# Optimization experiments

Measured on AMD Instinct MI355X. Metric: run time of the kernel, lower is better.

The kernel has to match this reference:

```python
import jax, jax.numpy as jnp
import numpy as np

PC = 512      # proposal_channels == conv_channels
INCH = 512    # in_channels of branch
B = 8
T = 64        # pyramid level length (feat_t) at order=0
TF = 256      # frame_level_feature length (clip_length)
KERNELS = [8, 16, 8, 4, 2, 2, 2]  # ConPoolingKernal
CLC = 498     # feature_lastclass channels (CLC + 2 == 500)
GROUPS = 32


def _gn(x, gamma, beta):
    # GroupNorm(32, C) over [B, C, L]
    Bb, C, L = x.shape
    xg = x.reshape(Bb, GROUPS, C // GROUPS, L)
    m = xg.mean(axis=(2, 3), keepdims=True)
    v = xg.var(axis=(2, 3), keepdims=True)
    xn = ((xg - m) * jax.lax.rsqrt(v + 1e-5)).reshape(Bb, C, L)
    return xn * gamma[None, :, None] + beta[None, :, None]


def _c1(x, w, b):
    # Unit1D kernel_shape=1: pointwise conv
    return jnp.einsum('bct,oc->bot', x, w) + b[None, :, None]


def _bmp(feat, segs):
    # BoundaryMaxPooling: first C/2 channels max-pooled over segs[...,0:2],
    # second C/2 over segs[...,2:4] (inclusive integer ranges, clamped).
    Bb, C, L = feat.shape
    C2 = C // 2
    pos = jnp.arange(L)
    def pool(f, s, e):
        s = jnp.clip(s, 0, L - 1)
        e = jnp.maximum(jnp.clip(e, 0, L - 1), s)
        mask = (pos[None, None, :] >= s[..., None]) & (pos[None, None, :] <= e[..., None])  # [B,T,L]
        return jnp.max(jnp.where(mask[:, None], f[:, :, None, :], -jnp.inf), axis=-1)  # [B,C2,T]
    return jnp.concatenate([pool(feat[:, :C2], segs[..., 0], segs[..., 1]),
                            pool(feat[:, C2:], segs[..., 2], segs[..., 3])], axis=1)


def _anchor_gather(feat, anc, K):
    # Vectorized per-anchor clamp/slice + nearest F.interpolate(size=K):
    # src index for output k of a slice [l, r] is l + floor(k * (r - l + 1) / K).
    Bb, C, L = feat.shape
    left = jnp.clip(anc[..., 0], 0, L)
    right = jnp.clip(anc[..., 1], 0, L)
    valid = right > left                      # empty slices -> zeros (torch branch)
    seglen = right + 1 - left
    k = jnp.arange(K)
    idx = jnp.clip(left[..., None] + (k[None, None, :] * seglen[..., None]) // K, 0, L - 1)  # [B,T,K]
    g = jax.vmap(lambda f, ix: f[:, ix])(feat, idx)   # [B,C,T,K]
    return g * valid[:, None, :, None].astype(feat.dtype)


def setup_inputs() -> dict:
    key = jax.random.key(0)
    ks = jax.random.split(key, 16)
    f32 = jnp.float32
    s = 0.02
    def w(k, shape):
        return jax.random.normal(k, shape, f32) * s
    inp = {}
    inp['feature'] = jax.random.normal(ks[0], (B, INCH, T), f32)
    inp['frame_level_feature'] = jax.random.normal(ks[1], (B, PC, TF), f32)
    inp['segments'] = jax.random.randint(ks[2], (B, T, 4), 0, T).astype(jnp.int32)
    inp['frame_segments'] = jax.random.randint(ks[3], (B, T, 4), 0, TF).astype(jnp.int32)
    inp['feature_lastclass'] = jax.random.normal(ks[4], (B, CLC, T), f32)
    inp['anchor'] = jnp.sort(jax.random.randint(ks[5], (B, T, 2), 0, T), axis=-1).astype(jnp.int32)
    inp['frame_anchor'] = jnp.sort(jax.random.randint(ks[6], (B, T, 2), 0, TF), axis=-1).astype(jnp.int32)
    inp['order'] = 0
    inp['LocResult_feature'] = jax.random.normal(ks[7], (B, 2, T), f32)
    inp['w_cur'] = w(ks[8], (PC, INCH)); inp['b_cur'] = jnp.zeros((PC,), f32)
    inp['g_cur'] = jnp.ones((PC,), f32); inp['be_cur'] = jnp.zeros((PC,), f32)
    inp['w_lr'] = w(ks[9], (2 * PC, INCH)); inp['b_lr'] = jnp.zeros((2 * PC,), f32)
    inp['g_lr'] = jnp.ones((2 * PC,), f32); inp['be_lr'] = jnp.zeros((2 * PC,), f32)
    inp['w_roi'] = w(ks[10], (PC, PC)); inp['b_roi'] = jnp.zeros((PC,), f32)
    inp['g_roi'] = jnp.ones((PC,), f32); inp['be_roi'] = jnp.zeros((PC,), f32)
    K1 = KERNELS[1]; K0 = KERNELS[0]
    inp['w_cp'] = w(ks[11], (PC, 2 * PC, K1)); inp['b_cp'] = jnp.zeros((PC,), f32)
    inp['w_cp0'] = w(ks[12], (PC, PC, K0)); inp['b_cp0'] = jnp.zeros((PC,), f32)
    CIN = 6 * PC + 500
    inp['w_prop'] = w(ks[13], (INCH, CIN)); inp['b_prop'] = jnp.zeros((INCH,), f32)
    inp['g_prop'] = jnp.ones((INCH,), f32); inp['be_prop'] = jnp.zeros((INCH,), f32)
    return inp


def reference(feature, frame_level_feature, segments, frame_segments, feature_lastclass,
              anchor, frame_anchor, order, LocResult_feature,
              w_cur, b_cur, g_cur, be_cur, w_lr, b_lr, g_lr, be_lr,
              w_roi, b_roi, g_roi, be_roi, w_cp, b_cp, w_cp0, b_cp0,
              w_prop, b_prop, g_prop, be_prop):
    relu = jax.nn.relu
    fm_short = relu(_gn(_c1(feature, w_cur, b_cur), g_cur, be_cur))           # [B,PC,T]
    feat_lr = relu(_gn(_c1(feature, w_lr, b_lr), g_lr, be_lr))                # [B,2PC,T]
    prop_feature = _bmp(feat_lr, segments)                                    # [B,2PC,T]
    prop_roi = relu(_gn(_c1(_bmp(frame_level_feature, frame_segments), w_roi, b_roi), g_roi, be_roi))
    K1 = KERNELS[order + 1]
    K0 = KERNELS[0]
    g1 = _anchor_gather(feat_lr, anchor, K1)                                  # [B,2PC,T,K1]
    con_feature = jnp.einsum('bctk,ock->bot', g1, w_cp) + b_cp[None, :, None]  # valid conv K1->1
    g0 = _anchor_gather(frame_level_feature, frame_anchor, K0)                # [B,PC,T,K0]
    frame_con = jnp.einsum('bctk,ock->bot', g0, w_cp0) + b_cp0[None, :, None]
    prop_con = relu(_gn(_c1(frame_con, w_roi, b_roi), g_roi, be_roi))
    cat = jnp.concatenate([prop_roi, prop_feature, fm_short, feature_lastclass,
                           con_feature, prop_con, LocResult_feature], axis=1)  # [B,6PC+500,T]
    out = relu(_gn(_c1(cat, w_prop, b_prop), g_prop, be_prop))                # [B,INCH,T]
    return (out, feat_lr)
```

## Files before the change

kernel.cpp:

```cpp
#include <hip/hip_runtime.h>
#include <math.h>

#define BB 8
#define CATP 3584
#define CAT_REAL 3572

typedef __attribute__((ext_vector_type(8))) short short8;
typedef __attribute__((ext_vector_type(4))) float f32x4;

__device__ inline ushort f2bf(float f) {
  union { float f; unsigned u; } x;
  x.f = f;
  return (ushort)((x.u + 0x7FFFu + ((x.u >> 16) & 1u)) >> 16);
}
__device__ inline float bf2f(unsigned us) {
  union { unsigned u; float f; } x;
  x.u = us << 16;
  return x.f;
}

__global__ __launch_bounds__(256) void cvt_weights_kernel(
    const float4* __restrict__ w_cur, const float4* __restrict__ w_lr,
    const float4* __restrict__ w_roi, uint2* __restrict__ Wcomb4,
    uint2* __restrict__ Wroi4, const float* __restrict__ w_prop,
    unsigned* __restrict__ Wprop) {
  int i = blockIdx.x * 256 + threadIdx.x;
  if (i < 262144) {
    const float4* S;
    uint2* D;
    if (i < 196608) {
      S = (i < 65536) ? (w_cur + i) : (w_lr + (i - 65536));
      D = Wcomb4 + i;
    } else {
      S = w_roi + (i - 196608);
      D = Wroi4 + (i - 196608);
    }
    const float4 v = *S;
    uint2 o;
    o.x = (unsigned)f2bf(v.x) | ((unsigned)f2bf(v.y) << 16);
    o.y = (unsigned)f2bf(v.z) | ((unsigned)f2bf(v.w) << 16);
    *D = o;
    return;
  }
  const int j = i - 262144;
  if (j >= 512 * 1792) return;
  const int p = j % 1792;
  const int o = j / 1792;
  const int c0 = 2 * p;
  unsigned pk = 0;
  if (c0 < CAT_REAL) {
    const float* w = w_prop + (size_t)o * CAT_REAL + c0;
    pk = (unsigned)f2bf(w[0]) | ((unsigned)f2bf(w[1]) << 16);
  }
  Wprop[(size_t)o * 1792 + p] = pk;
}

template <int C, int K>
__device__ void cpT_body(const float* __restrict__ W, ushort* __restrict__ D,
                         int o, float* tile ) {
  for (int c0 = 0; c0 < C; c0 += 256) {
    __syncthreads();
    for (int e = threadIdx.x; e < 256 * K; e += 256) {
      const int c = e / K, k = e % K;
      tile[c * (K + 1) + k] = W[(size_t)o * C * K + (size_t)c0 * K + e];
    }
    __syncthreads();
    for (int e = threadIdx.x; e < K * 128; e += 256) {
      const int k = e / 128, cp = e % 128;
      const float v0 = tile[(2 * cp) * (K + 1) + k];
      const float v1 = tile[(2 * cp + 1) * (K + 1) + k];
      const unsigned pk = (unsigned)f2bf(v0) | ((unsigned)f2bf(v1) << 16);
      *(unsigned*)(D + ((size_t)o * K + k) * C + c0 + 2 * cp) = pk;
    }
  }
}

__global__ __launch_bounds__(256) void cvt_cpT_kernel(
    const float* __restrict__ w_cp, ushort* __restrict__ WcpT,
    const float* __restrict__ w_cp0, ushort* __restrict__ Wcp0T) {
  __shared__ float tile[256 * 17];
  const int bid = blockIdx.x;
  if (bid < 512)
    cpT_body<1024, 16>(w_cp, WcpT, bid, tile);
  else
    cpT_body<512, 8>(w_cp0, Wcp0T, bid - 512, tile);
}

__global__ __launch_bounds__(256) void transpose_multi_kernel(
    const float* __restrict__ feature, const float* __restrict__ frame_feat,
    const float* __restrict__ lastcls, const float* __restrict__ locres,
    ushort* __restrict__ Ft, ushort* __restrict__ FfT,
    ushort* __restrict__ cat) {
  const int bid = blockIdx.x;
  const float* src;
  ushort* dst;
  int Cr, Cw, L, rs, co, cblk, lblk, b;
  if (bid < 64) {
    src = feature; dst = Ft; Cr = 512; Cw = 512; L = 64; rs = 512; co = 0;
    cblk = bid & 7; lblk = 0; b = bid >> 3;
  } else if (bid < 320) {
    const int r = bid - 64;
    src = frame_feat; dst = FfT; Cr = 512; Cw = 512; L = 256; rs = 512; co = 0;
    cblk = r & 7; lblk = (r >> 3) & 3; b = r >> 5;
  } else if (bid < 384) {
    const int r = bid - 320;
    src = lastcls; dst = cat; Cr = 498; Cw = 498; L = 64; rs = CATP; co = 2048;
    cblk = r & 7; lblk = 0; b = r >> 3;
  } else {
    const int r = bid - 384;
    src = locres; dst = cat; Cr = 2; Cw = 14; L = 64; rs = CATP; co = 3570;
    cblk = 0; lblk = 0; b = r;
  }
  __shared__ float tile[64 * 65];
  const int c0 = cblk * 64, l0 = lblk * 64;
  for (int e = threadIdx.x; e < 4096; e += 256) {
    const int cc = e >> 6, ll = e & 63;
    const int c = c0 + cc;
    tile[cc * 65 + ll] = (c < Cr) ? src[((size_t)b * Cr + c) * L + l0 + ll] : 0.f;
  }
  __syncthreads();
  for (int e = threadIdx.x; e < 4096; e += 256) {
    const int ll = e >> 6, cc = e & 63;
    const int c = c0 + cc;
    if (c < Cw)
      dst[((size_t)b * L + l0 + ll) * rs + co + c] = f2bf(tile[cc * 65 + ll]);
  }
}

__global__ __launch_bounds__(256) void gemm_gn_seg_kernel(
    int nblk0,
    const ushort* __restrict__ X0, const ushort* __restrict__ W0,
    const float* __restrict__ b0, const float* __restrict__ g0,
    const float* __restrict__ e0, int Kp0, int cs0, float* of0, int om0,
    ushort* co0, int cst0, int coff0,
    const ushort* __restrict__ X1, const ushort* __restrict__ W1,
    const float* __restrict__ b1, const float* __restrict__ g1,
    const float* __restrict__ e1, int Kp1, int cs1, float* of1, int om1,
    ushort* co1, int cst1, int coff1) {
  const int bx = blockIdx.x;
  const bool s1 = bx >= nblk0;
  const ushort* Xt = s1 ? X1 : X0;
  const ushort* Wb = s1 ? W1 : W0;
  const float* bias = s1 ? b1 : b0;
  const float* gamma = s1 ? g1 : g0;
  const float* beta = s1 ? e1 : e0;
  const int Kp = s1 ? Kp1 : Kp0;
  const int cpgShift = s1 ? cs1 : cs0;
  float* outF = s1 ? of1 : of0;
  const int outFM = s1 ? om1 : om0;
  ushort* catOut = s1 ? co1 : co0;
  const int catStride = s1 ? cst1 : cst0;
  const int chOff = s1 ? coff1 : coff0;
  const int o0 = (s1 ? bx - nblk0 : bx) * 64;

  const int b = blockIdx.y;
  const int w = threadIdx.x >> 6;
  const int lane = threadIdx.x & 63;
  const int l15 = lane & 15, l4 = lane >> 4;
  const int wk = Kp >> 2;
  const int kbeg = w * wk, kend = kbeg + wk;

  f32x4 acc[4][4] = {};
  const ushort* ap[4];
  const ushort* bp[4];
#pragma unroll
  for (int i = 0; i < 4; i++)
    ap[i] = Wb + (size_t)(o0 + i * 16 + l15) * Kp + l4 * 8;
#pragma unroll
  for (int j = 0; j < 4; j++)
    bp[j] = Xt + (size_t)(b * 64 + j * 16 + l15) * Kp + l4 * 8;

  for (int k = kbeg; k < kend; k += 32) {
    short8 a[4], x[4];
#pragma unroll
    for (int i = 0; i < 4; i++) a[i] = *(const short8*)(ap[i] + k);
#pragma unroll
    for (int j = 0; j < 4; j++) x[j] = *(const short8*)(bp[j] + k);
#pragma unroll
    for (int i = 0; i < 4; i++)
#pragma unroll
      for (int j = 0; j < 4; j++)
        acc[i][j] = __builtin_amdgcn_mfma_f32_16x16x32_bf16(a[i], x[j],
                                                            acc[i][j], 0, 0, 0);
  }

  __shared__ float red[64 * 65];
  for (int ww = 0; ww < 4; ww++) {
    __syncthreads();
    if (w == ww) {
#pragma unroll
      for (int i = 0; i < 4; i++)
#pragma unroll
        for (int j = 0; j < 4; j++)
#pragma unroll
          for (int r = 0; r < 4; r++) {
            const int m = i * 16 + l4 * 4 + r;
            const int n = j * 16 + l15;
            if (ww == 0)
              red[m * 65 + n] = acc[i][j][r] + bias[o0 + m];
            else
              red[m * 65 + n] += acc[i][j][r];
          }
    }
  }
  __syncthreads();

  const int cpg = 1 << cpgShift;
  const int ngroups = 64 >> cpgShift;
  __shared__ float rs[4], rss[4], gmean[4], grstd[4];
  for (int gi = 0; gi < ngroups; gi++) {
    float s = 0.f, ss = 0.f;
    const int nel = cpg << 6;
    for (int e = threadIdx.x; e < nel; e += 256) {
      const float v = red[((gi << cpgShift) + (e >> 6)) * 65 + (e & 63)];
      s += v;
      ss += v * v;
    }
#pragma unroll
    for (int off = 32; off > 0; off >>= 1) {
      s += __shfl_down(s, off);
      ss += __shfl_down(ss, off);
    }
    if (lane == 0) { rs[w] = s; rss[w] = ss; }
    __syncthreads();
    if (threadIdx.x == 0) {
      const float ts = rs[0] + rs[1] + rs[2] + rs[3];
      const float tss = rss[0] + rss[1] + rss[2] + rss[3];
      const float mean = ts / (float)nel;
      const float var = tss / (float)nel - mean * mean;
      gmean[gi] = mean;
      grstd[gi] = rsqrtf(var + 1e-5f);
    }
    __syncthreads();
  }

  if (outF) {
    for (int e = threadIdx.x; e < 4096; e += 256) {
      const int m = e >> 6, n = e & 63;
      const int gi = m >> cpgShift;
      const int c = o0 + m;
      float v = (red[m * 65 + n] - gmean[gi]) * grstd[gi] * gamma[c] + beta[c];
      v = fmaxf(v, 0.f);
      outF[((size_t)b * outFM + c) * 64 + n] = v;
    }
  }
  if (catOut) {
    for (int e = threadIdx.x; e < 4096; e += 256) {
      const int n = e >> 6, m = e & 63;
      const int gi = m >> cpgShift;
      const int c = o0 + m;
      float v = (red[m * 65 + n] - gmean[gi]) * grstd[gi] * gamma[c] + beta[c];
      v = fmaxf(v, 0.f);
      catOut[((size_t)(b * 64) + n) * catStride + chOff + c] = f2bf(v);
    }
  }
}

template <int C, int L>
__device__ void bmp_body(const ushort* __restrict__ Xt,
                         const int* __restrict__ segs, ushort* __restrict__ Y,
                         int rowStride, int chOff, float2 (*pmax)[512]) {
  constexpr int C2 = C / 2;
  constexpr int P2 = C2 / 2;
  constexpr int CH = P2 / 64;
  const int t = blockIdx.x;
  const int b = blockIdx.y;
  const int w = threadIdx.x >> 6;
  const int lane = threadIdx.x & 63;
  const int* sg = segs + ((size_t)b * 64 + t) * 4;
  const ushort* Xb = Xt + (size_t)b * L * C;
#pragma unroll
  for (int h = 0; h < 2; h++) {
    const int s = min(max(sg[2 * h], 0), L - 1);
    const int e = max(min(max(sg[2 * h + 1], 0), L - 1), s);
#pragma unroll
    for (int q = 0; q < CH; q++) {
      const int p = q * 64 + lane;
      const ushort* base = Xb + h * C2 + 2 * p;
      float a0 = -INFINITY, a1 = -INFINITY;
      float c0 = -INFINITY, c1 = -INFINITY;
      int l = s + w;
      for (; l + 4 <= e; l += 8) {
        const unsigned u0 = *(const unsigned*)(base + (size_t)l * C);
        const unsigned u1 = *(const unsigned*)(base + (size_t)(l + 4) * C);
        a0 = fmaxf(a0, bf2f(u0 & 0xffffu));
        a1 = fmaxf(a1, bf2f(u0 >> 16));
        c0 = fmaxf(c0, bf2f(u1 & 0xffffu));
        c1 = fmaxf(c1, bf2f(u1 >> 16));
      }
      if (l <= e) {
        const unsigned u0 = *(const unsigned*)(base + (size_t)l * C);
        a0 = fmaxf(a0, bf2f(u0 & 0xffffu));
        a1 = fmaxf(a1, bf2f(u0 >> 16));
      }
      pmax[w][h * P2 + p] = make_float2(fmaxf(a0, c0), fmaxf(a1, c1));
    }
  }
  __syncthreads();
  for (int idx = threadIdx.x; idx < 2 * P2; idx += 256) {
    float2 m = pmax[0][idx];
#pragma unroll
    for (int ww = 1; ww < 4; ww++) {
      const float2 v = pmax[ww][idx];
      m.x = fmaxf(m.x, v.x);
      m.y = fmaxf(m.y, v.y);
    }
    const unsigned o = (unsigned)f2bf(m.x) | ((unsigned)f2bf(m.y) << 16);
    *(unsigned*)(Y + ((size_t)(b * 64) + t) * rowStride + chOff + 2 * idx) = o;
  }
}

__global__ __launch_bounds__(256) void bmp_dual_kernel(
    const ushort* __restrict__ FlrT, const int* __restrict__ segments,
    ushort* __restrict__ cat, const ushort* __restrict__ FfT,
    const int* __restrict__ frame_segs, ushort* __restrict__ XbmpT) {
  __shared__ float2 pm[4][512];
  if (blockIdx.z == 0)
    bmp_body<1024, 64>(FlrT, segments, cat, CATP, 512, pm);
  else
    bmp_body<512, 256>(FfT, frame_segs, XbmpT, 512, 0, pm);
}

template <int Kf, int L, int Cin>
__device__ void anchor_mfma_body(const ushort* __restrict__ src,
                                 const int* __restrict__ anc,
                                 const ushort* __restrict__ Wt,
                                 float* __restrict__ P, int kz, float* red) {
  const int n0 = blockIdx.x * 64;
  const int b = blockIdx.y;
  const int w = threadIdx.x >> 6;
  const int lane = threadIdx.x & 63;
  const int l15 = lane & 15, l4 = lane >> 4;
  const int k = kz * 4 + w;

  const ushort* rp[4];
#pragma unroll
  for (int i = 0; i < 4; i++) {
    const int t = i * 16 + l15;
    const int a0 = anc[((size_t)b * 64 + t) * 2 + 0];
    const int a1 = anc[((size_t)b * 64 + t) * 2 + 1];
    const int left = min(max(a0, 0), L);
    const int right = min(max(a1, 0), L);
    const int seglen = right + 1 - left;
    const int ix = min(max(left + (k * seglen) / Kf, 0), L - 1);
    rp[i] = src + ((size_t)b * L + ix) * Cin + l4 * 8;
  }
  const ushort* wp[4];
#pragma unroll
  for (int j = 0; j < 4; j++)
    wp[j] = Wt + ((size_t)(n0 + j * 16 + l15) * Kf + k) * Cin + l4 * 8;

  f32x4 acc[4][4] = {};
  for (int c0 = 0; c0 < Cin; c0 += 32) {
    short8 a[4], bb[4];
#pragma unroll
    for (int i = 0; i < 4; i++) a[i] = *(const short8*)(rp[i] + c0);
#pragma unroll
    for (int j = 0; j < 4; j++) bb[j] = *(const short8*)(wp[j] + c0);
#pragma unroll
    for (int i = 0; i < 4; i++)
#pragma unroll
      for (int j = 0; j < 4; j++)
        acc[i][j] = __builtin_amdgcn_mfma_f32_16x16x32_bf16(a[i], bb[j],
                                                            acc[i][j], 0, 0, 0);
  }

  for (int ww = 0; ww < 4; ww++) {
    __syncthreads();
    if (w == ww) {
#pragma unroll
      for (int i = 0; i < 4; i++)
#pragma unroll
        for (int j = 0; j < 4; j++)
#pragma unroll
          for (int r = 0; r < 4; r++) {
            const int m = i * 16 + l4 * 4 + r;
            const int n = j * 16 + l15;
            if (ww == 0)
              red[m * 65 + n] = acc[i][j][r];
            else
              red[m * 65 + n] += acc[i][j][r];
          }
    }
  }
  __syncthreads();
  float* Pp = P + (((size_t)kz * BB + b) * 512 + n0) * 64;
  for (int e = threadIdx.x; e < 4096; e += 256) {
    const int n = e >> 6, m = e & 63;
    Pp[e] = red[m * 65 + n];
  }
}

__global__ __launch_bounds__(256) void anchor_mfma_dual_kernel(
    const ushort* __restrict__ FlrT, const int* __restrict__ anchor,
    const ushort* __restrict__ WcpT, float* __restrict__ P1,
    const ushort* __restrict__ FfT, const int* __restrict__ frame_anchor,
    const ushort* __restrict__ Wcp0T, float* __restrict__ P0) {
  __shared__ float red[64 * 65];
  const int z = blockIdx.z;
  if (z < 4)
    anchor_mfma_body<16, 64, 1024>(FlrT, anchor, WcpT, P1, z, red);
  else
    anchor_mfma_body<8, 256, 512>(FfT, frame_anchor, Wcp0T, P0, z - 4, red);
}

__device__ void anchor_reduce_body(const float* __restrict__ P, int ks,
                                   const float* __restrict__ bias,
                                   const int* __restrict__ anc, int L,
                                   ushort* __restrict__ Y, int rowStride,
                                   int chOff, float* tile, float* sval) {
  const int o0 = blockIdx.x * 64;
  const int b = blockIdx.y;
  if (threadIdx.x < 64) {
    const int t = threadIdx.x;
    const int a0 = anc[((size_t)b * 64 + t) * 2 + 0];
    const int a1 = anc[((size_t)b * 64 + t) * 2 + 1];
    const int left = min(max(a0, 0), L);
    const int right = min(max(a1, 0), L);
    sval[t] = (right > left) ? 1.f : 0.f;
  }
  __syncthreads();
  for (int e = threadIdx.x; e < 4096; e += 256) {
    const int nl = e >> 6, m = e & 63;
    const int n = o0 + nl;
    float s = 0.f;
    for (int z = 0; z < ks; z++)
      s += P[(((size_t)z * BB + b) * 512 + n) * 64 + m];
    tile[nl * 65 + m] = s * sval[m] + bias[n];
  }
  __syncthreads();
  for (int e = threadIdx.x; e < 4096; e += 256) {
    const int m = e >> 6, nl = e & 63;
    Y[((size_t)(b * 64) + m) * rowStride + chOff + o0 + nl] =
        f2bf(tile[nl * 65 + m]);
  }
}

__global__ __launch_bounds__(256) void anchor_reduce_dual_kernel(
    const float* __restrict__ P1, const float* __restrict__ b_cp,
    const int* __restrict__ anchor, ushort* __restrict__ cat,
    const float* __restrict__ P0, const float* __restrict__ b_cp0,
    const int* __restrict__ frame_anchor, ushort* __restrict__ FconT) {
  __shared__ float tile[64 * 65];
  __shared__ float sval[64];
  if (blockIdx.z == 0)
    anchor_reduce_body(P1, 4, b_cp, anchor, 64, cat, CATP, 2546, tile, sval);
  else
    anchor_reduce_body(P0, 2, b_cp0, frame_anchor, 256, FconT, 512, 0, tile, sval);
}

extern "C" void kernel_launch(void* const* d_in, const int* in_sizes, int n_in,
                              void* d_out, int out_size, void* d_ws,
                              size_t ws_size, hipStream_t stream) {
  const float* feature      = (const float*)d_in[0];
  const float* frame_feat   = (const float*)d_in[1];
  const int*   segments     = (const int*)d_in[2];
  const int*   frame_segs   = (const int*)d_in[3];
  const float* feat_lastcls = (const float*)d_in[4];
  const int*   anchor       = (const int*)d_in[5];
  const int*   frame_anchor = (const int*)d_in[6];
  const float* locres       = (const float*)d_in[8];
  const float* w_cur  = (const float*)d_in[9];
  const float* b_cur  = (const float*)d_in[10];
  const float* g_cur  = (const float*)d_in[11];
  const float* be_cur = (const float*)d_in[12];
  const float* w_lr   = (const float*)d_in[13];
  const float* b_lr   = (const float*)d_in[14];
  const float* g_lr   = (const float*)d_in[15];
  const float* be_lr  = (const float*)d_in[16];
  const float* w_roi  = (const float*)d_in[17];
  const float* b_roi  = (const float*)d_in[18];
  const float* g_roi  = (const float*)d_in[19];
  const float* be_roi = (const float*)d_in[20];
  const float* w_cp   = (const float*)d_in[21];
  const float* b_cp   = (const float*)d_in[22];
  const float* w_cp0  = (const float*)d_in[23];
  const float* b_cp0  = (const float*)d_in[24];
  const float* w_prop = (const float*)d_in[25];
  const float* b_prop = (const float*)d_in[26];
  const float* g_prop = (const float*)d_in[27];
  const float* be_prop= (const float*)d_in[28];

  float* out_main = (float*)d_out;
  float* feat_lr  = (float*)d_out + BB * 512 * 64;

  ushort* cat_t  = (ushort*)d_ws;
  ushort* Ft     = cat_t + 1835008;
  ushort* XbmpT  = Ft + 262144;
  ushort* FconT  = XbmpT + 262144;
  ushort* Wcomb  = FconT + 262144;
  ushort* Wroi   = Wcomb + 786432;
  ushort* Wprop  = Wroi + 262144;
  ushort* WcpT   = Wprop + 1835008;
  ushort* Wcp0T  = WcpT + 8388608;
  ushort* FlrT   = Wcp0T + 2097152;
  ushort* FfT    = FlrT + 524288;
  float*  P1     = (float*)(FfT + 1048576);
  float*  P0     = P1 + 1048576;

  cvt_weights_kernel<<<4608, 256, 0, stream>>>(
      (const float4*)w_cur, (const float4*)w_lr, (const float4*)w_roi,
      (uint2*)Wcomb, (uint2*)Wroi, w_prop, (unsigned*)Wprop);

  cvt_cpT_kernel<<<1024, 256, 0, stream>>>(w_cp, WcpT, w_cp0, Wcp0T);

  transpose_multi_kernel<<<392, 256, 0, stream>>>(
      feature, frame_feat, feat_lastcls, locres, Ft, FfT, cat_t);

  gemm_gn_seg_kernel<<<dim3(24, BB), 256, 0, stream>>>(
      8,
      Ft, Wcomb, b_cur, g_cur, be_cur, 512, 4, nullptr, 0, cat_t, CATP, 1536,
      Ft, Wcomb + 512 * 512, b_lr, g_lr, be_lr, 512, 5, feat_lr, 1024, FlrT,
      1024, 0);

  bmp_dual_kernel<<<dim3(64, BB, 2), 256, 0, stream>>>(
      FlrT, segments, cat_t, FfT, frame_segs, XbmpT);

  anchor_mfma_dual_kernel<<<dim3(8, BB, 6), 256, 0, stream>>>(
      FlrT, anchor, WcpT, P1, FfT, frame_anchor, Wcp0T, P0);

  anchor_reduce_dual_kernel<<<dim3(8, BB, 2), 256, 0, stream>>>(
      P1, b_cp, anchor, cat_t, P0, b_cp0, frame_anchor, FconT);

  gemm_gn_seg_kernel<<<dim3(16, BB), 256, 0, stream>>>(
      8,
      XbmpT, Wroi, b_roi, g_roi, be_roi, 512, 4, nullptr, 0, cat_t, CATP, 0,
      FconT, Wroi, b_roi, g_roi, be_roi, 512, 4, nullptr, 0, cat_t, CATP, 3058);

  gemm_gn_seg_kernel<<<dim3(8, BB), 256, 0, stream>>>(
      8,
      cat_t, Wprop, b_prop, g_prop, be_prop, CATP, 4, out_main, 512, nullptr,
      CATP, 0,
      cat_t, Wprop, b_prop, g_prop, be_prop, CATP, 4, nullptr, 0, nullptr,
      CATP, 0);
}
```

Measured before the change: 312.0 us.

## Pre-swizzle bf16 weights into MFMA fragment order and split anchor GEMM channels

Weight conversion kernels now write bf16 weights directly in the per-lane MFMA fragment layout, so each wave loads its A/B operands as contiguous 16-byte chunks instead of strided rows. The anchor MFMA kernel additionally splits the input-channel reduction into two halves, doubling grid z and the partial-sum buffers, with the reduce kernel summing twice as many slices. This is meant to improve memory coalescing of weight loads and increase parallelism, at the cost of more partial-sum traffic and workspace.

Result: no change. 308.6 us (-1.1%).

```diff
diff --git a/kernel.cpp b/kernel.cpp
--- a/kernel.cpp
+++ b/kernel.cpp
@@ -19,58 +19,85 @@
   return x.f;
 }
 
-__global__ __launch_bounds__(256) void cvt_weights_kernel(
-    const float4* __restrict__ w_cur, const float4* __restrict__ w_lr,
-    const float4* __restrict__ w_roi, uint2* __restrict__ Wcomb4,
-    uint2* __restrict__ Wroi4, const float* __restrict__ w_prop,
-    unsigned* __restrict__ Wprop) {
-  int i = blockIdx.x * 256 + threadIdx.x;
-  if (i < 262144) {
-    const float4* S;
-    uint2* D;
-    if (i < 196608) {
-      S = (i < 65536) ? (w_cur + i) : (w_lr + (i - 65536));
-      D = Wcomb4 + i;
-    } else {
-      S = w_roi + (i - 196608);
-      D = Wroi4 + (i - 196608);
-    }
-    const float4 v = *S;
-    uint2 o;
-    o.x = (unsigned)f2bf(v.x) | ((unsigned)f2bf(v.y) << 16);
-    o.y = (unsigned)f2bf(v.z) | ((unsigned)f2bf(v.w) << 16);
-    *D = o;
-    return;
-  }
-  const int j = i - 262144;
-  if (j >= 512 * 1792) return;
-  const int p = j % 1792;
-  const int o = j / 1792;
-  const int c0 = 2 * p;
-  unsigned pk = 0;
-  if (c0 < CAT_REAL) {
-    const float* w = w_prop + (size_t)o * CAT_REAL + c0;
-    pk = (unsigned)f2bf(w[0]) | ((unsigned)f2bf(w[1]) << 16);
-  }
-  Wprop[(size_t)o * 1792 + p] = pk;
-}
-
-template <int C, int K>
+__global__ __launch_bounds__(256) void cvt_wfrag_kernel(
+    const float* __restrict__ w_cur, const float* __restrict__ w_lr,
+    const float* __restrict__ w_roi, const float* __restrict__ w_prop,
+    ushort* __restrict__ Wcomb, ushort* __restrict__ Wroi,
+    ushort* __restrict__ Wprop) {
+  const int i = blockIdx.x * 256 + threadIdx.x;
+  const float* src;
+  ushort* dst;
+  int o, k8, Kc;
+  bool pad = false;
+  if (i < 98304) {
+    o = i >> 6; k8 = i & 63; Kc = 16;
+    src = (o < 512) ? (w_cur + (size_t)o * 512) : (w_lr + (size_t)(o - 512) * 512);
+    dst = Wcomb;
+  } else if (i < 131072) {
+    const int r = i - 98304;
+    o = r >> 6; k8 = r & 63; Kc = 16;
+    src = w_roi + (size_t)o * 512;
+    dst = Wroi;
+  } else {
+    const int r = i - 131072;
+    if (r >= 229376) return;
+    o = r / 448; k8 = r % 448; Kc = 112;
+    src = w_prop + (size_t)o * CAT_REAL;
+    dst = Wprop;
+    pad = true;
+  }
+  const int k = k8 * 8;
+  float v[8];
+  if (pad) {
+#pragma unroll
+    for (int q = 0; q < 8; q++) v[q] = (k + q < CAT_REAL) ? src[k + q] : 0.f;
+  } else {
+    const float4 f0 = *(const float4*)(src + k);
+    const float4 f1 = *(const float4*)(src + k + 4);
+    v[0] = f0.x; v[1] = f0.y; v[2] = f0.z; v[3] = f0.w;
+    v[4] = f1.x; v[5] = f1.y; v[6] = f1.z; v[7] = f1.w;
+  }
+  uint4 pk;
+  pk.x = (unsigned)f2bf(v[0]) | ((unsigned)f2bf(v[1]) << 16);
+  pk.y = (unsigned)f2bf(v[2]) | ((unsigned)f2bf(v[3]) << 16);
+  pk.z = (unsigned)f2bf(v[4]) | ((unsigned)f2bf(v[5]) << 16);
+  pk.w = (unsigned)f2bf(v[6]) | ((unsigned)f2bf(v[7]) << 16);
+  const int ot = o >> 6, ii = (o >> 4) & 3, l15 = o & 15;
+  const int kc = k8 >> 2, l4 = k8 & 3;
+  const size_t flat =
+      ((((size_t)ot * Kc + kc) * 4 + ii) * 64 + l4 * 16 + l15) * 8;
+  *(uint4*)(dst + flat) = pk;
+}
+
+template <int Cin, int Kf>
 __device__ void cpT_body(const float* __restrict__ W, ushort* __restrict__ D,
                          int o, float* tile ) {
-  for (int c0 = 0; c0 < C; c0 += 256) {
+  const int nt = o >> 6, j = (o >> 4) & 3, l15 = o & 15;
+  for (int c0 = 0; c0 < Cin; c0 += 256) {
     __syncthreads();
-    for (int e = threadIdx.x; e < 256 * K; e += 256) {
-      const int c = e / K, k = e % K;
-      tile[c * (K + 1) + k] = W[(size_t)o * C * K + (size_t)c0 * K + e];
+    for (int e = threadIdx.x; e < 256 * Kf; e += 256) {
+      const int c = e / Kf, k = e % Kf;
+      tile[c * (Kf + 1) + k] = W[((size_t)o * Cin + c0) * Kf + e];
     }
     __syncthreads();
-    for (int e = threadIdx.x; e < K * 128; e += 256) {
-      const int k = e / 128, cp = e % 128;
-      const float v0 = tile[(2 * cp) * (K + 1) + k];
-      const float v1 = tile[(2 * cp + 1) * (K + 1) + k];
-      const unsigned pk = (unsigned)f2bf(v0) | ((unsigned)f2bf(v1) << 16);
-      *(unsigned*)(D + ((size_t)o * K + k) * C + c0 + 2 * cp) = pk;
+    for (int e = threadIdx.x; e < Kf * 32; e += 256) {
+      const int k = e >> 5, c8 = e & 31;
+      const int cl = c8 * 8;
+      const int c = c0 + cl;
+      uint4 pk;
+      pk.x = (unsigned)f2bf(tile[(cl + 0) * (Kf + 1) + k]) |
+             ((unsigned)f2bf(tile[(cl + 1) * (Kf + 1) + k]) << 16);
+      pk.y = (unsigned)f2bf(tile[(cl + 2) * (Kf + 1) + k]) |
+             ((unsigned)f2bf(tile[(cl + 3) * (Kf + 1) + k]) << 16);
+      pk.z = (unsigned)f2bf(tile[(cl + 4) * (Kf + 1) + k]) |
+             ((unsigned)f2bf(tile[(cl + 5) * (Kf + 1) + k]) << 16);
+      pk.w = (unsigned)f2bf(tile[(cl + 6) * (Kf + 1) + k]) |
+             ((unsigned)f2bf(tile[(cl + 7) * (Kf + 1) + k]) << 16);
+      const int cc = c >> 5, l4 = (c >> 3) & 3;
+      const size_t flat =
+          ((((size_t)nt * Kf + k) * (Cin >> 5) + cc) * 4 + j) * 512 +
+          (l4 * 16 + l15) * 8;
+      *(uint4*)(D + flat) = pk;
     }
   }
 }
@@ -161,19 +188,18 @@
   const int kbeg = w * wk, kend = kbeg + wk;
 
   f32x4 acc[4][4] = {};
-  const ushort* ap[4];
+  const ushort* wbase = Wb + (size_t)(o0 >> 6) * (Kp >> 5) * 2048 + lane * 8;
   const ushort* bp[4];
-#pragma unroll
-  for (int i = 0; i < 4; i++)
-    ap[i] = Wb + (size_t)(o0 + i * 16 + l15) * Kp + l4 * 8;
 #pragma unroll
   for (int j = 0; j < 4; j++)
     bp[j] = Xt + (size_t)(b * 64 + j * 16 + l15) * Kp + l4 * 8;
 
   for (int k = kbeg; k < kend; k += 32) {
+    const int kc = k >> 5;
     short8 a[4], x[4];
 #pragma unroll
-    for (int i = 0; i < 4; i++) a[i] = *(const short8*)(ap[i] + k);
+    for (int i = 0; i < 4; i++)
+      a[i] = *(const short8*)(wbase + ((size_t)kc * 4 + i) * 512);
 #pragma unroll
     for (int j = 0; j < 4; j++) x[j] = *(const short8*)(bp[j] + k);
 #pragma unroll
@@ -325,13 +351,15 @@
 __device__ void anchor_mfma_body(const ushort* __restrict__ src,
                                  const int* __restrict__ anc,
                                  const ushort* __restrict__ Wt,
-                                 float* __restrict__ P, int kz, float* red) {
-  const int n0 = blockIdx.x * 64;
+                                 float* __restrict__ P, int slice, float* red) {
+  const int nt = blockIdx.x;
   const int b = blockIdx.y;
   const int w = threadIdx.x >> 6;
   const int lane = threadIdx.x & 63;
   const int l15 = lane & 15, l4 = lane >> 4;
+  const int kz = slice >> 1, chalf = slice & 1;
   const int k = kz * 4 + w;
+  const int cbase = chalf * (Cin / 2);
 
   const ushort* rp[4];
 #pragma unroll
@@ -343,20 +371,19 @@
     const int right = min(max(a1, 0), L);
     const int seglen = right + 1 - left;
     const int ix = min(max(left + (k * seglen) / Kf, 0), L - 1);
-    rp[i] = src + ((size_t)b * L + ix) * Cin + l4 * 8;
-  }
-  const ushort* wp[4];
-#pragma unroll
-  for (int j = 0; j < 4; j++)
-    wp[j] = Wt + ((size_t)(n0 + j * 16 + l15) * Kf + k) * Cin + l4 * 8;
+    rp[i] = src + ((size_t)b * L + ix) * Cin + cbase + l4 * 8;
+  }
+  const ushort* wb = Wt + (size_t)(nt * Kf + k) * (Cin >> 5) * 2048 + lane * 8;
 
   f32x4 acc[4][4] = {};
-  for (int c0 = 0; c0 < Cin; c0 += 32) {
+  for (int c0 = 0; c0 < Cin / 2; c0 += 32) {
+    const int cc = (cbase + c0) >> 5;
     short8 a[4], bb[4];
 #pragma unroll
     for (int i = 0; i < 4; i++) a[i] = *(const short8*)(rp[i] + c0);
 #pragma unroll
-    for (int j = 0; j < 4; j++) bb[j] = *(const short8*)(wp[j] + c0);
+    for (int j = 0; j < 4; j++)
+      bb[j] = *(const short8*)(wb + ((size_t)cc * 4 + j) * 512);
 #pragma unroll
     for (int i = 0; i < 4; i++)
 #pragma unroll
@@ -384,7 +411,7 @@
     }
   }
   __syncthreads();
-  float* Pp = P + (((size_t)kz * BB + b) * 512 + n0) * 64;
+  float* Pp = P + (((size_t)slice * BB + b) * 512 + nt * 64) * 64;
   for (int e = threadIdx.x; e < 4096; e += 256) {
     const int n = e >> 6, m = e & 63;
     Pp[e] = red[m * 65 + n];
@@ -398,10 +425,10 @@
     const ushort* __restrict__ Wcp0T, float* __restrict__ P0) {
   __shared__ float red[64 * 65];
   const int z = blockIdx.z;
-  if (z < 4)
+  if (z < 8)
     anchor_mfma_body<16, 64, 1024>(FlrT, anchor, WcpT, P1, z, red);
   else
-    anchor_mfma_body<8, 256, 512>(FfT, frame_anchor, Wcp0T, P0, z - 4, red);
+    anchor_mfma_body<8, 256, 512>(FfT, frame_anchor, Wcp0T, P0, z - 8, red);
 }
 
 __device__ void anchor_reduce_body(const float* __restrict__ P, int ks,
@@ -444,9 +471,9 @@
   __shared__ float tile[64 * 65];
   __shared__ float sval[64];
   if (blockIdx.z == 0)
-    anchor_reduce_body(P1, 4, b_cp, anchor, 64, cat, CATP, 2546, tile, sval);
+    anchor_reduce_body(P1, 8, b_cp, anchor, 64, cat, CATP, 2546, tile, sval);
   else
-    anchor_reduce_body(P0, 2, b_cp0, frame_anchor, 256, FconT, 512, 0, tile, sval);
+    anchor_reduce_body(P0, 4, b_cp0, frame_anchor, 256, FconT, 512, 0, tile, sval);
 }
 
 extern "C" void kernel_launch(void* const* d_in, const int* in_sizes, int n_in,
@@ -496,11 +523,10 @@
   ushort* FlrT   = Wcp0T + 2097152;
   ushort* FfT    = FlrT + 524288;
   float*  P1     = (float*)(FfT + 1048576);
-  float*  P0     = P1 + 1048576;
-
-  cvt_weights_kernel<<<4608, 256, 0, stream>>>(
-      (const float4*)w_cur, (const float4*)w_lr, (const float4*)w_roi,
-      (uint2*)Wcomb, (uint2*)Wroi, w_prop, (unsigned*)Wprop);
+  float*  P0     = P1 + 2097152;
+
+  cvt_wfrag_kernel<<<1408, 256, 0, stream>>>(
+      w_cur, w_lr, w_roi, w_prop, Wcomb, Wroi, Wprop);
 
   cvt_cpT_kernel<<<1024, 256, 0, stream>>>(w_cp, WcpT, w_cp0, Wcp0T);
 
@@ -516,7 +542,7 @@
   bmp_dual_kernel<<<dim3(64, BB, 2), 256, 0, stream>>>(
       FlrT, segments, cat_t, FfT, frame_segs, XbmpT);
 
-  anchor_mfma_dual_kernel<<<dim3(8, BB, 6), 256, 0, stream>>>(
+  anchor_mfma_dual_kernel<<<dim3(8, BB, 12), 256, 0, stream>>>(
       FlrT, anchor, WcpT, P1, FfT, frame_anchor, Wcp0T, P0);
 
   anchor_reduce_dual_kernel<<<dim3(8, BB, 2), 256, 0, stream>>>(
```
